# Optimization experiments

Measured on AMD Instinct MI355X. Metric: run time of the kernel, lower is better.

The kernel has to match this reference:

```python
import jax, jax.numpy as jnp
import numpy as np

N_SRC = 100000
N_DST = 100000
N_EDGES = 640000
D = 128
D_OUT = 128


def setup_inputs() -> dict:
    key = jax.random.key(0)
    k1, k2, k3, k4, k5, k6 = jax.random.split(key, 6)
    h_src = jax.random.normal(k1, (N_SRC, D), dtype=jnp.float32)
    h_dst = jax.random.normal(k2, (N_DST, D), dtype=jnp.float32)
    src_idx = jax.random.randint(k3, (N_EDGES,), 0, N_SRC, dtype=jnp.int32)
    dst_idx = jax.random.randint(k4, (N_EDGES,), 0, N_DST, dtype=jnp.int32)
    W = jax.random.normal(k5, (2 * D, D_OUT), dtype=jnp.float32) * 0.05
    b = jax.random.normal(k6, (D_OUT,), dtype=jnp.float32) * 0.05
    return {"h_src": h_src, "h_dst": h_dst, "src_idx": src_idx,
            "dst_idx": dst_idx, "W": W, "b": b}


def reference(h_src, h_dst, src_idx, dst_idx, W, b):
    # copy_u: gather source features along edges -> [E, D]
    msgs = h_src[src_idx]
    # mean aggregation per destination node (segment mean)
    summed = jax.ops.segment_sum(msgs, dst_idx, num_segments=N_DST)  # [N_dst, D]
    deg = jax.ops.segment_sum(jnp.ones((N_EDGES,), dtype=h_src.dtype),
                              dst_idx, num_segments=N_DST)  # [N_dst]
    h_N = summed / jnp.maximum(deg, 1.0)[:, None]
    # concat self + neighbor mean, then linear projection
    h_total = jnp.concatenate([h_dst, h_N], axis=1)  # [N_dst, 2D]
    return h_total @ W + b
```

## Files before the change

### kernel.cpp

```cpp
#include <hip/hip_runtime.h>

#define D 128
#define N_SRC 100000
#define N_DST 100000
#define N_EDGES 640000

#define SCAN_BLK 1024
#define N_SCAN_BLOCKS ((N_DST + SCAN_BLK - 1) / SCAN_BLK)

#define HIST_BLOCKS ((N_EDGES + 255) / 256)
#define CVT_BLOCKS  ((N_SRC * D / 8) / 256)
#define PACKW_BLOCKS 128

typedef __attribute__((ext_vector_type(8))) short s8v;
typedef __attribute__((ext_vector_type(4))) float f32x4;

__device__ __forceinline__ unsigned short f2bf(float f) {
    unsigned int u = __float_as_uint(f);
    u += 0x7fffu + ((u >> 16) & 1u);
    return (unsigned short)(u >> 16);
}

__device__ __forceinline__ unsigned int pk2(float a, float b) {
    return (unsigned int)f2bf(a) | ((unsigned int)f2bf(b) << 16);
}

__global__ __launch_bounds__(256) void prep(
    const int* __restrict__ dst_idx, int* __restrict__ counts,
    const float* __restrict__ h_src, unsigned int* __restrict__ A32,
    const float* __restrict__ W, unsigned short* __restrict__ Bp)
{
    const int blk = blockIdx.x;
    const int tid = threadIdx.x;
    if (blk < HIST_BLOCKS) {
        int e = blk * 256 + tid;
        if (e < N_EDGES) atomicAdd(&counts[dst_idx[e]], 1);
    } else if (blk < HIST_BLOCKS + CVT_BLOCKS) {
        int id = (blk - HIST_BLOCKS) * 256 + tid;
        size_t e = (size_t)id * 8;
        const float4* p = (const float4*)(h_src + e);
        float4 x = p[0], y = p[1];
        uint4 o;
        o.x = pk2(x.x, x.y); o.y = pk2(x.z, x.w);
        o.z = pk2(y.x, y.y); o.w = pk2(y.z, y.w);
        int r = id >> 4;
        int c = (id & 15) * 8;
        *(uint4*)(A32 + (size_t)r * 128 + (c >> 1)) = o;
    } else {
        int id = (blk - HIST_BLOCKS - CVT_BLOCKS) * 256 + tid;
        if (id < 32768) {
            int j = id & 7;
            int l = (id >> 3) & 63;
            int t = (id >> 9) & 7;
            int s = id >> 12;
            int k = s * 32 + (l >> 4) * 8 + j;
            int n = t * 16 + (l & 15);
            Bp[id] = f2bf(W[k * D + n]);
        }
    }
}


__global__ __launch_bounds__(256) void scan_blocks(
    const int* __restrict__ counts, int* __restrict__ row_start,
    int* __restrict__ block_sums)
{
    __shared__ int sh[256];
    const int tid = threadIdx.x;
    const int base = blockIdx.x * SCAN_BLK + tid * 4;
    int v[4];
    int local = 0;
#pragma unroll
    for (int k = 0; k < 4; k++) {
        int idx = base + k;
        v[k] = (idx < N_DST) ? counts[idx] : 0;
        local += v[k];
    }
    sh[tid] = local;
    __syncthreads();
    for (int off = 1; off < 256; off <<= 1) {
        int t = (tid >= off) ? sh[tid - off] : 0;
        __syncthreads();
        sh[tid] += t;
        __syncthreads();
    }
    int run = (tid == 0) ? 0 : sh[tid - 1];
    if (tid == 255) block_sums[blockIdx.x] = sh[255];
#pragma unroll
    for (int k = 0; k < 4; k++) {
        int idx = base + k;
        if (idx < N_DST) row_start[idx] = run;
        run += v[k];
    }
}

__global__ __launch_bounds__(256) void add_offsets(
    int* __restrict__ row_start, const int* __restrict__ block_sums,
    int* __restrict__ cursor)
{
    __shared__ int sh[128];
    const int tid = threadIdx.x;
    if (tid < 128) sh[tid] = (tid < N_SCAN_BLOCKS) ? block_sums[tid] : 0;
    __syncthreads();
    for (int off = 1; off < 128; off <<= 1) {
        int t = (tid < 128 && tid >= off) ? sh[tid - off] : 0;
        __syncthreads();
        if (tid < 128) sh[tid] += t;
        __syncthreads();
    }
    int i = blockIdx.x * 256 + tid;
    if (i < N_DST) {
        int blk = i / SCAN_BLK;
        int off = (blk == 0) ? 0 : sh[blk - 1];
        int v = row_start[i] + off;
        row_start[i] = v;
        cursor[i] = v;
    }
    if (i == 0) row_start[N_DST] = N_EDGES;
}

__global__ __launch_bounds__(256) void scatter_perm(
    const int* __restrict__ src_idx, const int* __restrict__ dst_idx,
    int* __restrict__ cursor, int* __restrict__ edge_src)
{
    int e = blockIdx.x * 256 + threadIdx.x;
    if (e < N_EDGES) {
        int d = dst_idx[e];
        int pos = atomicAdd(&cursor[d], 1);
        edge_src[pos] = src_idx[e];
    }
}

__global__ __launch_bounds__(256) void aggregate(
    const unsigned short* __restrict__ hs16,
    const int* __restrict__ row_start,
    const int* __restrict__ edge_src, unsigned int* __restrict__ A32)
{
    const int wave = threadIdx.x >> 6;
    const int grp = (threadIdx.x >> 4) & 3;
    const int gl = threadIdx.x & 15;
    const int row = blockIdx.x * 16 + wave * 4 + grp;
    const int start = row_start[row];
    const int deg = row_start[row + 1] - start;
    float acc[8] = {0.f, 0.f, 0.f, 0.f, 0.f, 0.f, 0.f, 0.f};
    for (int base = 0; base < deg; base += 8) {
        int j = base + (gl & 7);
        int myid = edge_src[start + min(j, deg - 1)];
#pragma unroll
        for (int t = 0; t < 8; t++) {
            int s = __shfl(myid, t, 16);
            uint4 u = *(const uint4*)(hs16 + (size_t)s * 256 + gl * 8);
            float m = ((base + t) < deg) ? 1.f : 0.f;
            acc[0] = fmaf(__uint_as_float(u.x << 16), m, acc[0]);
            acc[1] = fmaf(__uint_as_float(u.x & 0xffff0000u), m, acc[1]);
            acc[2] = fmaf(__uint_as_float(u.y << 16), m, acc[2]);
            acc[3] = fmaf(__uint_as_float(u.y & 0xffff0000u), m, acc[3]);
            acc[4] = fmaf(__uint_as_float(u.z << 16), m, acc[4]);
            acc[5] = fmaf(__uint_as_float(u.z & 0xffff0000u), m, acc[5]);
            acc[6] = fmaf(__uint_as_float(u.w << 16), m, acc[6]);
            acc[7] = fmaf(__uint_as_float(u.w & 0xffff0000u), m, acc[7]);
        }
    }
    const float inv = 1.0f / fmaxf((float)deg, 1.0f);
    uint4 o;
    o.x = pk2(acc[0] * inv, acc[1] * inv);
    o.y = pk2(acc[2] * inv, acc[3] * inv);
    o.z = pk2(acc[4] * inv, acc[5] * inv);
    o.w = pk2(acc[6] * inv, acc[7] * inv);
    *(uint4*)(A32 + (size_t)row * 128 + 64 + gl * 4) = o;
}

__global__ __launch_bounds__(256, 2) void mfma_gemm(
    const float* __restrict__ h_dst,
    const unsigned short* __restrict__ A,
    const unsigned short* __restrict__ Bp,
    const float* __restrict__ bias,
    float* __restrict__ out)
{
    __shared__ uint4 Bs4[2048];
    unsigned short* Bs = (unsigned short*)Bs4;
    const int tid = threadIdx.x;
    const int wave = tid >> 6;
    const int lane = tid & 63;
    const int quad = lane >> 4;
    const int lr = lane & 15;
    const int row0 = blockIdx.x * 128 + wave * 32;

    const int r0 = min(row0 + lr, N_DST - 1);
    const int r1 = min(row0 + 16 + lr, N_DST - 1);

    {
        const uint4* src = (const uint4*)Bp;
#pragma unroll
        for (int i = 0; i < 8; i++)
            Bs4[tid + i * 256] = src[tid + i * 256];
    }

    const float* p0 = h_dst + (size_t)r0 * D + quad * 8;
    const float* p1 = h_dst + (size_t)r1 * D + quad * 8;
    const unsigned short* q0 = A + (size_t)r0 * 256 + 128 + quad * 8;
    const unsigned short* q1 = A + (size_t)r1 * 256 + 128 + quad * 8;

    float4 x0[4], y0[4], x1[4], y1[4];
    s8v an0[4], an1[4];
#pragma unroll
    for (int s = 0; s < 4; s++) {
        x0[s] = *(const float4*)(p0 + s * 32);
        y0[s] = *(const float4*)(p0 + s * 32 + 4);
        x1[s] = *(const float4*)(p1 + s * 32);
        y1[s] = *(const float4*)(p1 + s * 32 + 4);
        an0[s] = *(const s8v*)(q0 + s * 32);
        an1[s] = *(const s8v*)(q1 + s * 32);
    }
    s8v af0[4], af1[4];
#pragma unroll
    for (int s = 0; s < 4; s++) {
        unsigned short u0[8], u1[8];
        u0[0]=f2bf(x0[s].x); u0[1]=f2bf(x0[s].y); u0[2]=f2bf(x0[s].z); u0[3]=f2bf(x0[s].w);
        u0[4]=f2bf(y0[s].x); u0[5]=f2bf(y0[s].y); u0[6]=f2bf(y0[s].z); u0[7]=f2bf(y0[s].w);
        u1[0]=f2bf(x1[s].x); u1[1]=f2bf(x1[s].y); u1[2]=f2bf(x1[s].z); u1[3]=f2bf(x1[s].w);
        u1[4]=f2bf(y1[s].x); u1[5]=f2bf(y1[s].y); u1[6]=f2bf(y1[s].z); u1[7]=f2bf(y1[s].w);
        af0[s] = *(s8v*)u0;
        af1[s] = *(s8v*)u1;
    }

    f32x4 acc0[8], acc1[8];
#pragma unroll
    for (int t = 0; t < 8; t++) {
        acc0[t] = (f32x4){0.f, 0.f, 0.f, 0.f};
        acc1[t] = (f32x4){0.f, 0.f, 0.f, 0.f};
    }

    __syncthreads();

#pragma unroll
    for (int s = 0; s < 4; s++) {
#pragma unroll
        for (int t = 0; t < 8; t++) {
            s8v bf = *(const s8v*)(Bs + ((s * 8 + t) * 64 + lane) * 8);
            acc0[t] = __builtin_amdgcn_mfma_f32_16x16x32_bf16(af0[s], bf, acc0[t], 0, 0, 0);
            acc1[t] = __builtin_amdgcn_mfma_f32_16x16x32_bf16(af1[s], bf, acc1[t], 0, 0, 0);
        }
    }

    __syncthreads();

    {
        const uint4* src = (const uint4*)(Bp + 16384);
#pragma unroll
        for (int i = 0; i < 8; i++)
            Bs4[tid + i * 256] = src[tid + i * 256];
    }
    __syncthreads();

#pragma unroll
    for (int s = 0; s < 4; s++) {
#pragma unroll
        for (int t = 0; t < 8; t++) {
            s8v bf = *(const s8v*)(Bs + ((s * 8 + t) * 64 + lane) * 8);
            acc0[t] = __builtin_amdgcn_mfma_f32_16x16x32_bf16(an0[s], bf, acc0[t], 0, 0, 0);
            acc1[t] = __builtin_amdgcn_mfma_f32_16x16x32_bf16(an1[s], bf, acc1[t], 0, 0, 0);
        }
    }

#pragma unroll
    for (int t = 0; t < 8; t++) {
        float bv = bias[t * 16 + lr];
#pragma unroll
        for (int r = 0; r < 4; r++) {
            int rowa = row0 + quad * 4 + r;
            int rowb = row0 + 16 + quad * 4 + r;
            if (rowa < N_DST) out[(size_t)rowa * D + t * 16 + lr] = acc0[t][r] + bv;
            if (rowb < N_DST) out[(size_t)rowb * D + t * 16 + lr] = acc1[t][r] + bv;
        }
    }
}

extern "C" void kernel_launch(void* const* d_in, const int* in_sizes, int n_in,
                              void* d_out, int out_size, void* d_ws, size_t ws_size,
                              hipStream_t stream) {
    const float* h_src  = (const float*)d_in[0];
    const float* h_dst  = (const float*)d_in[1];
    const int* src_idx  = (const int*)d_in[2];
    const int* dst_idx  = (const int*)d_in[3];
    const float* W      = (const float*)d_in[4];
    const float* b      = (const float*)d_in[5];
    float* out = (float*)d_out;

    unsigned short* Bp = (unsigned short*)d_ws;
    int* ws_i          = (int*)((char*)d_ws + 65536);
    int* row_start     = ws_i;
    int* cursor        = row_start + (N_DST + 1);
    int* counts        = cursor + N_DST;
    int* block_sums    = counts + N_DST;
    int* edge_src      = block_sums + N_SCAN_BLOCKS;

    hipMemsetAsync(counts, 0, (size_t)N_DST * sizeof(int), stream);

    prep<<<HIST_BLOCKS + CVT_BLOCKS + PACKW_BLOCKS, 256, 0, stream>>>(
        dst_idx, counts, h_src, (unsigned int*)d_out, W, Bp);

    scan_blocks<<<N_SCAN_BLOCKS, 256, 0, stream>>>(counts, row_start, block_sums);
    add_offsets<<<(N_DST + 255) / 256, 256, 0, stream>>>(row_start, block_sums, cursor);
    scatter_perm<<<(N_EDGES + 255) / 256, 256, 0, stream>>>(src_idx, dst_idx, cursor, edge_src);

    aggregate<<<N_DST / 16, 256, 0, stream>>>(
        (const unsigned short*)d_out, row_start, edge_src, (unsigned int*)d_out);

    int gemm_blocks = (N_DST + 127) / 128;
    mfma_gemm<<<gemm_blocks, 256, 0, stream>>>(
        h_dst, (const unsigned short*)d_out, Bp, b, out);
}
```

Measured before the change: 264.4 us.

## Fuse neighbor aggregation with MFMA projection via workspace bf16 mirror

Adds a fused kernel in which each 64-row block gathers and mean-aggregates neighbor bf16 features into LDS, then runs both halves of the projection GEMM with bf16 MFMA and writes the output directly. The bf16 copy of h_src moves from the output buffer to a dense workspace region with a 64-word row stride, so the intermediate h_N round trip through global memory and one kernel launch are removed. The old path stays as a fallback when the workspace is too small. The cost is heavier per-block LDS use and register pressure, which could lower occupancy for the latency-bound gather.

```diff
diff --git a/kernel.cpp b/kernel.cpp
--- a/kernel.cpp
+++ b/kernel.cpp
@@ -27,7 +27,8 @@
 
 __global__ __launch_bounds__(256) void prep(
     const int* __restrict__ dst_idx, int* __restrict__ counts,
-    const float* __restrict__ h_src, unsigned int* __restrict__ A32,
+    const float* __restrict__ h_src, unsigned int* __restrict__ mir32,
+    int mir_stride32,
     const float* __restrict__ W, unsigned short* __restrict__ Bp)
 {
     const int blk = blockIdx.x;
@@ -45,7 +46,7 @@
         o.z = pk2(y.x, y.y); o.w = pk2(y.z, y.w);
         int r = id >> 4;
         int c = (id & 15) * 8;
-        *(uint4*)(A32 + (size_t)r * 128 + (c >> 1)) = o;
+        *(uint4*)(mir32 + (size_t)r * mir_stride32 + (c >> 1)) = o;
     } else {
         int id = (blk - HIST_BLOCKS - CVT_BLOCKS) * 256 + tid;
         if (id < 32768) {
@@ -130,6 +131,141 @@
         edge_src[pos] = src_idx[e];
     }
 }
+
+__global__ __launch_bounds__(256, 3) void fused_ag(
+    const float* __restrict__ h_dst,
+    const unsigned short* __restrict__ mir,
+    const int* __restrict__ row_start,
+    const int* __restrict__ edge_src,
+    const unsigned short* __restrict__ Bp,
+    const float* __restrict__ bias,
+    float* __restrict__ out)
+{
+    __shared__ uint4 Bs4[2048];
+    __shared__ uint4 hN4[1024];
+    unsigned short* Bs = (unsigned short*)Bs4;
+    char* hN = (char*)hN4;
+
+    const int tid = threadIdx.x;
+    const int wave = tid >> 6;
+    const int lane = tid & 63;
+    const int quad = lane >> 4;
+    const int lr = lane & 15;
+    const int rw0 = blockIdx.x * 64 + wave * 16;
+
+    {
+        const uint4* src = (const uint4*)Bp;
+#pragma unroll
+        for (int i = 0; i < 8; i++)
+            Bs4[tid + i * 256] = src[tid + i * 256];
+    }
+
+    const int r0 = min(rw0 + lr, N_DST - 1);
+    const float* p0 = h_dst + (size_t)r0 * D + quad * 8;
+    float4 x0[4], y0[4];
+#pragma unroll
+    for (int s = 0; s < 4; s++) {
+        x0[s] = *(const float4*)(p0 + s * 32);
+        y0[s] = *(const float4*)(p0 + s * 32 + 4);
+    }
+
+#pragma unroll
+    for (int i = 0; i < 4; i++) {
+        int rl = wave * 16 + i * 4 + quad;
+        int row = min(blockIdx.x * 64 + rl, N_DST - 1);
+        int start = row_start[row];
+        int deg = row_start[row + 1] - start;
+        float a[8] = {0.f, 0.f, 0.f, 0.f, 0.f, 0.f, 0.f, 0.f};
+        for (int base = 0; base < deg; base += 8) {
+            int j = base + (lr & 7);
+            int myid = edge_src[start + min(j, deg - 1)];
+#pragma unroll
+            for (int t = 0; t < 8; t++) {
+                int s = __shfl(myid, t, 16);
+                uint4 u = *(const uint4*)(mir + (size_t)s * 128 + lr * 8);
+                float m = ((base + t) < deg) ? 1.f : 0.f;
+                a[0] = fmaf(__uint_as_float(u.x << 16), m, a[0]);
+                a[1] = fmaf(__uint_as_float(u.x & 0xffff0000u), m, a[1]);
+                a[2] = fmaf(__uint_as_float(u.y << 16), m, a[2]);
+                a[3] = fmaf(__uint_as_float(u.y & 0xffff0000u), m, a[3]);
+                a[4] = fmaf(__uint_as_float(u.z << 16), m, a[4]);
+                a[5] = fmaf(__uint_as_float(u.z & 0xffff0000u), m, a[5]);
+                a[6] = fmaf(__uint_as_float(u.w << 16), m, a[6]);
+                a[7] = fmaf(__uint_as_float(u.w & 0xffff0000u), m, a[7]);
+            }
+        }
+        float inv = 1.0f / fmaxf((float)deg, 1.0f);
+        uint4 o;
+        o.x = pk2(a[0] * inv, a[1] * inv);
+        o.y = pk2(a[2] * inv, a[3] * inv);
+        o.z = pk2(a[4] * inv, a[5] * inv);
+        o.w = pk2(a[6] * inv, a[7] * inv);
+        int ba = (rl * 256 + lr * 16) ^ ((rl & 7) << 4);
+        *(uint4*)(hN + ba) = o;
+    }
+
+    s8v af0[4];
+#pragma unroll
+    for (int s = 0; s < 4; s++) {
+        unsigned short u0[8];
+        u0[0]=f2bf(x0[s].x); u0[1]=f2bf(x0[s].y); u0[2]=f2bf(x0[s].z); u0[3]=f2bf(x0[s].w);
+        u0[4]=f2bf(y0[s].x); u0[5]=f2bf(y0[s].y); u0[6]=f2bf(y0[s].z); u0[7]=f2bf(y0[s].w);
+        af0[s] = *(s8v*)u0;
+    }
+
+    f32x4 acc[8];
+#pragma unroll
+    for (int t = 0; t < 8; t++) acc[t] = (f32x4){0.f, 0.f, 0.f, 0.f};
+
+    __syncthreads();
+
+#pragma unroll
+    for (int s = 0; s < 4; s++) {
+#pragma unroll
+        for (int t = 0; t < 8; t++) {
+            s8v bf = *(const s8v*)(Bs + ((s * 8 + t) * 64 + lane) * 8);
+            acc[t] = __builtin_amdgcn_mfma_f32_16x16x32_bf16(af0[s], bf, acc[t], 0, 0, 0);
+        }
+    }
+
+    __syncthreads();
+
+    {
+        const uint4* src = (const uint4*)(Bp + 16384);
+#pragma unroll
+        for (int i = 0; i < 8; i++)
+            Bs4[tid + i * 256] = src[tid + i * 256];
+    }
+
+    s8v an[4];
+#pragma unroll
+    for (int s = 0; s < 4; s++) {
+        int rl = wave * 16 + lr;
+        int ba = (rl * 256 + s * 64 + quad * 16) ^ ((rl & 7) << 4);
+        an[s] = *(const s8v*)(hN + ba);
+    }
+    __syncthreads();
+
+#pragma unroll
+    for (int s = 0; s < 4; s++) {
+#pragma unroll
+        for (int t = 0; t < 8; t++) {
+            s8v bf = *(const s8v*)(Bs + ((s * 8 + t) * 64 + lane) * 8);
+            acc[t] = __builtin_amdgcn_mfma_f32_16x16x32_bf16(an[s], bf, acc[t], 0, 0, 0);
+        }
+    }
+
+#pragma unroll
+    for (int t = 0; t < 8; t++) {
+        float bv = bias[t * 16 + lr];
+#pragma unroll
+        for (int r = 0; r < 4; r++) {
+            int row = rw0 + quad * 4 + r;
+            if (row < N_DST) out[(size_t)row * D + t * 16 + lr] = acc[t][r] + bv;
+        }
+    }
+}
+
 
 __global__ __launch_bounds__(256) void aggregate(
     const unsigned short* __restrict__ hs16,
@@ -295,19 +431,31 @@
     int* block_sums    = counts + N_DST;
     int* edge_src      = block_sums + N_SCAN_BLOCKS;
 
+    size_t int_bytes = (size_t)(N_DST + 1 + N_DST + N_DST + N_SCAN_BLOCKS + N_EDGES) * 4;
+    size_t mir_off   = (65536 + int_bytes + 255) & ~(size_t)255;
+    size_t ws_need   = mir_off + (size_t)N_SRC * D * 2;
+    const bool fused_ok = ws_size >= ws_need;
+
     hipMemsetAsync(counts, 0, (size_t)N_DST * sizeof(int), stream);
 
-    prep<<<HIST_BLOCKS + CVT_BLOCKS + PACKW_BLOCKS, 256, 0, stream>>>(
-        dst_idx, counts, h_src, (unsigned int*)d_out, W, Bp);
-
-    scan_blocks<<<N_SCAN_BLOCKS, 256, 0, stream>>>(counts, row_start, block_sums);
-    add_offsets<<<(N_DST + 255) / 256, 256, 0, stream>>>(row_start, block_sums, cursor);
-    scatter_perm<<<(N_EDGES + 255) / 256, 256, 0, stream>>>(src_idx, dst_idx, cursor, edge_src);
-
-    aggregate<<<N_DST / 16, 256, 0, stream>>>(
-        (const unsigned short*)d_out, row_start, edge_src, (unsigned int*)d_out);
-
-    int gemm_blocks = (N_DST + 127) / 128;
-    mfma_gemm<<<gemm_blocks, 256, 0, stream>>>(
-        h_dst, (const unsigned short*)d_out, Bp, b, out);
-}
+    if (fused_ok) {
+        unsigned short* mir = (unsigned short*)((char*)d_ws + mir_off);
+        prep<<<HIST_BLOCKS + CVT_BLOCKS + PACKW_BLOCKS, 256, 0, stream>>>(
+            dst_idx, counts, h_src, (unsigned int*)mir, 64, W, Bp);
+        scan_blocks<<<N_SCAN_BLOCKS, 256, 0, stream>>>(counts, row_start, block_sums);
+        add_offsets<<<(N_DST + 255) / 256, 256, 0, stream>>>(row_start, block_sums, cursor);
+        scatter_perm<<<(N_EDGES + 255) / 256, 256, 0, stream>>>(src_idx, dst_idx, cursor, edge_src);
+        fused_ag<<<(N_DST + 63) / 64, 256, 0, stream>>>(
+            h_dst, mir, row_start, edge_src, Bp, b, out);
+    } else {
+        prep<<<HIST_BLOCKS + CVT_BLOCKS + PACKW_BLOCKS, 256, 0, stream>>>(
+            dst_idx, counts, h_src, (unsigned int*)d_out, 128, W, Bp);
+        scan_blocks<<<N_SCAN_BLOCKS, 256, 0, stream>>>(counts, row_start, block_sums);
+        add_offsets<<<(N_DST + 255) / 256, 256, 0, stream>>>(row_start, block_sums, cursor);
+        scatter_perm<<<(N_EDGES + 255) / 256, 256, 0, stream>>>(src_idx, dst_idx, cursor, edge_src);
+        aggregate<<<N_DST / 16, 256, 0, stream>>>(
+            (const unsigned short*)d_out, row_start, edge_src, (unsigned int*)d_out);
+        mfma_gemm<<<(N_DST + 127) / 128, 256, 0, stream>>>(
+            h_dst, (const unsigned short*)d_out, Bp, b, out);
+    }
+}
```

After: 260.7 us. No clear change (-1.4%).
